# Kernel tuning notes

Hardware: AMD Instinct MI355X
Metric: run time of the kernel (lower is better)

Reference implementation:

```python
import jax, jax.numpy as jnp
import numpy as np

K = 32  # num_nearest_neighbors

def silu(x):
    return x * jax.nn.sigmoid(x)

def setup_inputs() -> dict:
    key = jax.random.key(0)
    ks = jax.random.split(key, 10)
    b, n, d, m = 4, 2048, 64, 16
    e_in = 2 * d + 1  # 129 = fourier*2 + dim*2 + edge_dim + 1
    std = 0.001  # init_eps normal init on Linear weights
    inp = {
        "feats": jax.random.normal(ks[0], (b, n, d), dtype=jnp.float32),
        "coors": jax.random.normal(ks[1], (b, n, 3), dtype=jnp.float32),
        # edge_mlp: Linear(129,258) -> SiLU -> Linear(258,16) -> SiLU
        "ew1": jax.random.normal(ks[2], (e_in, 2 * e_in), dtype=jnp.float32) * std,
        "eb1": jnp.zeros((2 * e_in,), dtype=jnp.float32),
        "ew2": jax.random.normal(ks[3], (2 * e_in, m), dtype=jnp.float32) * std,
        "eb2": jnp.zeros((m,), dtype=jnp.float32),
        # coors_mlp: Linear(16,64) -> SiLU -> Linear(64,1)
        "cw1": jax.random.normal(ks[4], (m, 4 * m), dtype=jnp.float32) * std,
        "cb1": jnp.zeros((4 * m,), dtype=jnp.float32),
        "cw2": jax.random.normal(ks[5], (4 * m, 1), dtype=jnp.float32) * std,
        "cb2": jnp.zeros((1,), dtype=jnp.float32),
        # node_mlp: Linear(80,128) -> SiLU -> Linear(128,64)
        "nw1": jax.random.normal(ks[6], (d + m, 2 * d), dtype=jnp.float32) * std,
        "nb1": jnp.zeros((2 * d,), dtype=jnp.float32),
        "nw2": jax.random.normal(ks[7], (2 * d, d), dtype=jnp.float32) * std,
        "nb2": jnp.zeros((d,), dtype=jnp.float32),
    }
    return inp


def reference(feats, coors, ew1, eb1, ew2, eb2, cw1, cb1, cw2, cb2, nw1, nb1, nw2, nb2):
    b, n, d = feats.shape
    # pairwise relative coords / squared distances: [b,n,n,3], [b,n,n]
    rel = coors[:, :, None, :] - coors[:, None, :, :]
    dist2 = jnp.sum(rel * rel, axis=-1)
    # k nearest neighbors (smallest squared distance)
    _, idx = jax.lax.top_k(-dist2, K)  # idx: [b,n,K]
    bi = jnp.arange(b)[:, None, None]
    ii = jnp.arange(n)[None, :, None]
    rel_k = rel[bi, ii, idx]                # [b,n,K,3]
    dist_k = dist2[bi, ii, idx][..., None]  # [b,n,K,1]
    feats_j = feats[bi, idx]                # [b,n,K,d]
    feats_i = jnp.broadcast_to(feats[:, :, None, :], feats_j.shape)
    # edge MLP
    edge_in = jnp.concatenate([feats_i, feats_j, dist_k], axis=-1)  # [b,n,K,2d+1]
    h = silu(edge_in @ ew1 + eb1)
    m_ij = silu(h @ ew2 + eb2)  # [b,n,K,m]
    # coordinate update
    coor_w = (silu(m_ij @ cw1 + cb1) @ cw2 + cb2)[..., 0]  # [b,n,K]
    coors_out = jnp.einsum('bik,bikc->bic', coor_w, rel_k) + coors
    # node update (sum pooling over neighbors)
    m_i = jnp.sum(m_ij, axis=-2)  # [b,n,m]
    node_in = jnp.concatenate([feats, m_i], axis=-1)
    node_out = silu(node_in @ nw1 + nb1) @ nw2 + nb2 + feats
    return (node_out, coors_out)
```

## Files before the change

kernel.cpp:

```cpp
#include <hip/hip_runtime.h>
#include <math.h>

#define NB 4
#define NN 2048
#define ND 64
#define NM 16
#define NK 32
#define EIN 129
#define EH 258
#define CHD 64
#define NHD 128
#define PQS 288
#define XS 96
#define KNN_BLOCKS (NB * NN / 4)
#define PREP_BLOCKS 92

typedef __attribute__((ext_vector_type(8))) short short8;
typedef __attribute__((ext_vector_type(4))) float f32x4;
typedef __attribute__((ext_vector_type(4))) int intx4;

__device__ __forceinline__ float fast_silu(float x) {
    return x * __builtin_amdgcn_rcpf(1.f + __expf(-x));
}

__device__ __forceinline__ short f2bf(float f) {
    union { float f; unsigned u; } v; v.f = f;
    unsigned r = v.u + 0x7FFFu + ((v.u >> 16) & 1u);
    return (short)(r >> 16);
}

__device__ __forceinline__ float bf2f(short s) {
    union { unsigned u; float f; } v;
    v.u = ((unsigned)(unsigned short)s) << 16;
    return v.f;
}

__device__ __forceinline__ unsigned cvt_pk_bf16(float lo, float hi) {
    unsigned r;
    asm("v_cvt_pk_bf16_f32 %0, %1, %2" : "=v"(r) : "v"(lo), "v"(hi));
    return r;
}

__device__ __forceinline__ unsigned umin_u(unsigned a, unsigned b) { return a < b ? a : b; }
__device__ __forceinline__ unsigned umax_u(unsigned a, unsigned b) { return a > b ? a : b; }

__global__ __launch_bounds__(256) void pk_kernel(
    const float* __restrict__ coors, int* __restrict__ idx_out,
    const float* __restrict__ ew1, const float* __restrict__ ew2, const float* __restrict__ eb1,
    const float* __restrict__ cw1,
    const float* __restrict__ nw1, const float* __restrict__ nw2,
    float* __restrict__ w1pad, float* __restrict__ eb1pad,
    short* __restrict__ W2T, short* __restrict__ W1F, short* __restrict__ cw1T,
    short* __restrict__ nw1F, short* __restrict__ nw2F) {
    const int tid = threadIdx.x;

    if (blockIdx.x >= KNN_BLOCKS) {
        const int blk = blockIdx.x - KNN_BLOCKS;
        if (blk < 72) {
            const int kk = blk & 1, ct = (blk >> 1) % 18, half = blk / 36;
            for (int t = tid; t < 512; t += 256) {
                const int l = t >> 3, i = t & 7;
                const int er = l & 15, grp = l >> 4;
                const int k = kk * 32 + grp * 8 + i;
                const int col = ct * 16 + er;
                const int row = half * 64 + k;
                W1F[blk * 512 + t] = (col < EH) ? f2bf(ew1[row * EH + col]) : (short)0;
            }
        } else if (blk == 72) {
            for (int c = tid; c < PQS; c += 256) {
                w1pad[c] = (c < EH) ? ew1[128 * EH + c] : 0.f;
                eb1pad[c] = (c < EH) ? eb1[c] : 0.f;
            }
        } else if (blk < 89) {
            const int t = blk - 73;
            for (int k = tid; k < PQS; k += 256)
                W2T[t * PQS + k] = (k < EH) ? f2bf(ew2[k * NM + t]) : (short)0;
        } else if (blk == 89) {
            for (int t2 = tid; t2 < CHD * NM; t2 += 256) {
                const int h = t2 >> 4, t = t2 & 15;
                cw1T[t2] = f2bf(cw1[t * CHD + h]);
            }
        } else if (blk == 90) {
            for (int t = tid; t < 24 * 512; t += 256) {
                const int f = t >> 9, t2 = t & 511;
                const int ct = f / 3, kk = f % 3;
                const int l = t2 >> 3, i = t2 & 7;
                const int er = l & 15, grp = l >> 4;
                const int k = kk * 32 + grp * 8 + i;
                const int col = ct * 16 + er;
                nw1F[t] = (k < 80) ? f2bf(nw1[k * NHD + col]) : (short)0;
            }
        } else {
            for (int t = tid; t < 16 * 512; t += 256) {
                const int f = t >> 9, t2 = t & 511;
                const int ct = f >> 2, kk = f & 3;
                const int l = t2 >> 3, i = t2 & 7;
                const int er = l & 15, grp = l >> 4;
                const int k = kk * 32 + grp * 8 + i;
                const int col = ct * 16 + er;
                nw2F[t] = f2bf(nw2[k * ND + col]);
            }
        }
        return;
    }

    const int wg = ((blockIdx.x & 7) << 8) | (blockIdx.x >> 3);
    const int wv = tid >> 6;
    const int lane = tid & 63;
    const int row = wg * 4 + wv;
    const int b = row >> 11;
    const int i = row & (NN - 1);
    const float* cb = coors + (size_t)b * NN * 3;
    const float cix = cb[i * 3 + 0], ciy = cb[i * 3 + 1], ciz = cb[i * 3 + 2];

    unsigned k[32];
    #pragma unroll
    for (int t = 0; t < 32; ++t) {
        int j = lane + 64 * t;
        const float* cj = cb + (size_t)j * 3;
        float dx = cix - cj[0];
        float dy = ciy - cj[1];
        float dz = ciz - cj[2];
        float d = dx * dx + dy * dy + dz * dz;
        union { float f; unsigned u; } v; v.f = d;
        k[t] = (v.u & 0xFFFFF800u) | (unsigned)j;
    }

    #pragma unroll
    for (int size = 2; size <= 32; size <<= 1) {
        #pragma unroll
        for (int stride = size >> 1; stride > 0; stride >>= 1) {
            #pragma unroll
            for (int t = 0; t < 32; ++t) {
                int p = t ^ stride;
                if (p > t) {
                    const bool up = ((t & size) == 0);
                    unsigned lo = umin_u(k[t], k[p]);
                    unsigned hi = umax_u(k[t], k[p]);
                    k[t] = up ? lo : hi;
                    k[p] = up ? hi : lo;
                }
            }
        }
    }

    #pragma unroll
    for (int off = 1; off < 64; off <<= 1) {
        unsigned pr[32];
        #pragma unroll
        for (int t = 0; t < 32; ++t) pr[t] = __shfl_xor(k[31 - t], off);
        #pragma unroll
        for (int t = 0; t < 32; ++t) k[t] = umin_u(k[t], pr[t]);
        #pragma unroll
        for (int s = 16; s > 0; s >>= 1) {
            #pragma unroll
            for (int t = 0; t < 32; ++t) {
                if ((t & s) == 0) {
                    const int p = t | s;
                    unsigned lo = umin_u(k[t], k[p]);
                    unsigned hi = umax_u(k[t], k[p]);
                    k[t] = lo; k[p] = hi;
                }
            }
        }
    }

    if (lane == 0) {
        intx4* op = (intx4*)(idx_out + (size_t)row * NK);
        #pragma unroll
        for (int q = 0; q < 8; ++q) {
            intx4 v;
            v[0] = (int)(k[q * 4 + 0] & 2047u);
            v[1] = (int)(k[q * 4 + 1] & 2047u);
            v[2] = (int)(k[q * 4 + 2] & 2047u);
            v[3] = (int)(k[q * 4 + 3] & 2047u);
            op[q] = v;
        }
    }
}

__global__ __launch_bounds__(256) void pq_kernel(const float* __restrict__ feats,
                                                 const short* __restrict__ W1F,
                                                 const float* __restrict__ eb1pad,
                                                 short* __restrict__ P,
                                                 short* __restrict__ Q,
                                                 short* __restrict__ xbuf) {
    const int wv = threadIdx.x >> 6, lane = threadIdx.x & 63;
    const int er = lane & 15, grp = lane >> 4;
    const int wid = blockIdx.x * 4 + wv;
    const int mt = wid / 18, ct = wid % 18;
    const int nb = mt * 16;

    short8 a[2];
    #pragma unroll
    for (int kk = 0; kk < 2; ++kk) {
        const float* fp = feats + (size_t)(nb + er) * ND + kk * 32 + grp * 8;
        f32x4 f0 = *(const f32x4*)fp;
        f32x4 f1 = *(const f32x4*)(fp + 4);
        union { intx4 iv; short8 s; } u;
        u.iv[0] = cvt_pk_bf16(f0[0], f0[1]);
        u.iv[1] = cvt_pk_bf16(f0[2], f0[3]);
        u.iv[2] = cvt_pk_bf16(f1[0], f1[1]);
        u.iv[3] = cvt_pk_bf16(f1[2], f1[3]);
        a[kk] = u.s;
    }

    if (ct == 0) {
        short* xr = xbuf + (size_t)(nb + er) * XS;
        *(short8*)(xr + 0 * 32 + grp * 8) = a[0];
        *(short8*)(xr + 1 * 32 + grp * 8) = a[1];
        if (grp == 0) {
            const short8 z8 = {0, 0, 0, 0, 0, 0, 0, 0};
            *(short8*)(xr + 80) = z8;
            *(short8*)(xr + 88) = z8;
        }
    }

    const short8* WF = (const short8*)W1F;
    short8 bP0 = WF[((0 * 18 + ct) * 2 + 0) * 64 + lane];
    short8 bP1 = WF[((0 * 18 + ct) * 2 + 1) * 64 + lane];
    short8 bQ0 = WF[((1 * 18 + ct) * 2 + 0) * 64 + lane];
    short8 bQ1 = WF[((1 * 18 + ct) * 2 + 1) * 64 + lane];

    f32x4 accP = {0.f, 0.f, 0.f, 0.f};
    f32x4 accQ = {0.f, 0.f, 0.f, 0.f};
    accP = __builtin_amdgcn_mfma_f32_16x16x32_bf16(a[0], bP0, accP, 0, 0, 0);
    accP = __builtin_amdgcn_mfma_f32_16x16x32_bf16(a[1], bP1, accP, 0, 0, 0);
    accQ = __builtin_amdgcn_mfma_f32_16x16x32_bf16(a[0], bQ0, accQ, 0, 0, 0);
    accQ = __builtin_amdgcn_mfma_f32_16x16x32_bf16(a[1], bQ1, accQ, 0, 0, 0);

    const float bias = eb1pad[ct * 16 + er];
    #pragma unroll
    for (int r = 0; r < 4; ++r) {
        const int node = nb + grp * 4 + r;
        P[(size_t)node * PQS + ct * 16 + er] = f2bf(accP[r] + bias);
        Q[(size_t)node * PQS + ct * 16 + er] = f2bf(accQ[r]);
    }
}

__global__ __launch_bounds__(256) void edge_kernel(
    const float* __restrict__ coors, const int* __restrict__ idx,
    const short* __restrict__ P, const short* __restrict__ Q,
    const float* __restrict__ w1pad, const short* __restrict__ W2T,
    const float* __restrict__ eb2,
    const short* __restrict__ cw1T, const float* __restrict__ cb1,
    const float* __restrict__ cw2, const float* __restrict__ cb2,
    float* __restrict__ coors_out, short* __restrict__ xbuf) {

    __shared__ __align__(16) short mtl[4][NK][NM];

    const int tid = threadIdx.x;
    const int wg = ((blockIdx.x & 7) << 8) | (blockIdx.x >> 3);
    const int wv = tid >> 6, lane = tid & 63;
    const int er = lane & 15, grp = lane >> 4;
    const int gi = wg * 4 + wv;
    const int b = gi >> 11;

    const int j0 = idx[gi * NK + er];
    const int j1 = idx[gi * NK + 16 + er];
    const float ci0 = coors[gi * 3 + 0], ci1 = coors[gi * 3 + 1], ci2 = coors[gi * 3 + 2];
    const float* cj0p = coors + (size_t)(b * NN + j0) * 3;
    const float* cj1p = coors + (size_t)(b * NN + j1) * 3;
    const float r0x = ci0 - cj0p[0], r0y = ci1 - cj0p[1], r0z = ci2 - cj0p[2];
    const float r1x = ci0 - cj1p[0], r1y = ci1 - cj1p[1], r1z = ci2 - cj1p[2];
    const float d0 = r0x * r0x + r0y * r0y + r0z * r0z;
    const float d1 = r1x * r1x + r1y * r1y + r1z * r1z;

    const short8* Pr8 = (const short8*)(P + (size_t)gi * PQS);
    const short8* Q0 = (const short8*)(Q + (size_t)(b * NN + j0) * PQS);
    const short8* Q1 = (const short8*)(Q + (size_t)(b * NN + j1) * PQS);
    const short8* w2row = (const short8*)(W2T + er * PQS);
    const f32x4* w14 = (const f32x4*)w1pad;

    short8 qb0a[9], qb1a[9];
    #pragma unroll
    for (int kk = 0; kk < 9; ++kk) {
        qb0a[kk] = Q0[kk * 4 + grp];
        qb1a[kk] = Q1[kk * 4 + grp];
    }

    f32x4 acc0 = {0.f, 0.f, 0.f, 0.f};
    f32x4 acc1 = {0.f, 0.f, 0.f, 0.f};
    #pragma unroll
    for (int kk = 0; kk < 9; ++kk) {
        short8 bf = w2row[kk * 4 + grp];
        short8 pb = Pr8[kk * 4 + grp];
        f32x4 w0 = w14[kk * 8 + grp * 2];
        f32x4 w1 = w14[kk * 8 + grp * 2 + 1];
        float wf[8] = {w0[0], w0[1], w0[2], w0[3], w1[0], w1[1], w1[2], w1[3]};
        float pf[8];
        #pragma unroll
        for (int i = 0; i < 8; ++i) pf[i] = bf2f(pb[i]);
        float h0[8], h1[8];
        #pragma unroll
        for (int i = 0; i < 8; ++i) {
            h0[i] = fast_silu(fmaf(d0, wf[i], pf[i]) + bf2f(qb0a[kk][i]));
            h1[i] = fast_silu(fmaf(d1, wf[i], pf[i]) + bf2f(qb1a[kk][i]));
        }
        union { intx4 iv; short8 s; } u0, u1;
        u0.iv[0] = cvt_pk_bf16(h0[0], h0[1]);
        u0.iv[1] = cvt_pk_bf16(h0[2], h0[3]);
        u0.iv[2] = cvt_pk_bf16(h0[4], h0[5]);
        u0.iv[3] = cvt_pk_bf16(h0[6], h0[7]);
        u1.iv[0] = cvt_pk_bf16(h1[0], h1[1]);
        u1.iv[1] = cvt_pk_bf16(h1[2], h1[3]);
        u1.iv[2] = cvt_pk_bf16(h1[4], h1[5]);
        u1.iv[3] = cvt_pk_bf16(h1[6], h1[7]);
        acc0 = __builtin_amdgcn_mfma_f32_16x16x32_bf16(u0.s, bf, acc0, 0, 0, 0);
        acc1 = __builtin_amdgcn_mfma_f32_16x16x32_bf16(u1.s, bf, acc1, 0, 0, 0);
    }

    const float eb2v = eb2[er];
    float m0[4], m1[4];
    #pragma unroll
    for (int r = 0; r < 4; ++r) {
        m0[r] = fast_silu(acc0[r] + eb2v);
        m1[r] = fast_silu(acc1[r] + eb2v);
    }

    float s = m0[0] + m0[1] + m0[2] + m0[3] + m1[0] + m1[1] + m1[2] + m1[3];
    s += __shfl_xor(s, 16);
    s += __shfl_xor(s, 32);
    if (lane < NM) xbuf[(size_t)gi * XS + ND + er] = f2bf(s);

    #pragma unroll
    for (int r = 0; r < 4; ++r) {
        mtl[wv][grp * 4 + r][er] = f2bf(m0[r]);
        mtl[wv][16 + grp * 4 + r][er] = f2bf(m1[r]);
    }
    __syncthreads();

    const short8 zero8 = {0, 0, 0, 0, 0, 0, 0, 0};
    short8 afr[4];
    #pragma unroll
    for (int mt = 0; mt < 4; ++mt)
        afr[mt] = (grp < 2) ? *(const short8*)(cw1T + (mt * 16 + er) * NM + grp * 8) : zero8;

    float cwv[2];
    #pragma unroll
    for (int nt = 0; nt < 2; ++nt) {
        short8 bfr = (grp < 2) ? *(const short8*)&mtl[wv][nt * 16 + er][grp * 8] : zero8;
        float partial = 0.f;
        #pragma unroll
        for (int mt = 0; mt < 4; ++mt) {
            f32x4 dz = {0.f, 0.f, 0.f, 0.f};
            dz = __builtin_amdgcn_mfma_f32_16x16x32_bf16(afr[mt], bfr, dz, 0, 0, 0);
            f32x4 cb1v = *(const f32x4*)(cb1 + mt * 16 + grp * 4);
            f32x4 cw2v = *(const f32x4*)(cw2 + mt * 16 + grp * 4);
            #pragma unroll
            for (int r = 0; r < 4; ++r)
                partial += fast_silu(dz[r] + cb1v[r]) * cw2v[r];
        }
        partial += __shfl_xor(partial, 16);
        partial += __shfl_xor(partial, 32);
        cwv[nt] = partial + cb2[0];
    }

    float wx = cwv[0] * r0x + cwv[1] * r1x;
    float wy = cwv[0] * r0y + cwv[1] * r1y;
    float wz = cwv[0] * r0z + cwv[1] * r1z;
    #pragma unroll
    for (int off = 1; off < 16; off <<= 1) {
        wx += __shfl_xor(wx, off);
        wy += __shfl_xor(wy, off);
        wz += __shfl_xor(wz, off);
    }
    if (lane == 0) {
        coors_out[gi * 3 + 0] = ci0 + wx;
        coors_out[gi * 3 + 1] = ci1 + wy;
        coors_out[gi * 3 + 2] = ci2 + wz;
    }
}

__global__ __launch_bounds__(256) void node_kernel(
    const short* __restrict__ xbuf,
    const short* __restrict__ nw1F, const float* __restrict__ nb1,
    const short* __restrict__ nw2F, const float* __restrict__ nb2,
    const float* __restrict__ feats, float* __restrict__ node_out) {
    __shared__ __align__(16) short hl[16 * 128];
    const int tid = threadIdx.x;
    const int wv = tid >> 6, lane = tid & 63;
    const int er = lane & 15, grp = lane >> 4;
    const int nb = blockIdx.x * 16;

    short8 a[3];
    #pragma unroll
    for (int kk = 0; kk < 3; ++kk)
        a[kk] = *(const short8*)(xbuf + (size_t)(nb + er) * XS + kk * 32 + grp * 8);

    #pragma unroll
    for (int c2 = 0; c2 < 2; ++c2) {
        const int ct = wv * 2 + c2;
        f32x4 acc = {0.f, 0.f, 0.f, 0.f};
        #pragma unroll
        for (int kk = 0; kk < 3; ++kk)
            acc = __builtin_amdgcn_mfma_f32_16x16x32_bf16(
                a[kk], *(const short8*)(nw1F + (ct * 3 + kk) * 512 + lane * 8), acc, 0, 0, 0);
        const float b1 = nb1[ct * 16 + er];
        #pragma unroll
        for (int r = 0; r < 4; ++r) {
            const int row = grp * 4 + r;
            int byte = row * 256 + (ct * 16 + er) * 2;
            byte ^= (row & 7) << 4;
            *(short*)((char*)hl + byte) = f2bf(fast_silu(acc[r] + b1));
        }
    }
    __syncthreads();

    short8 a2[4];
    #pragma unroll
    for (int kk = 0; kk < 4; ++kk) {
        int byte = er * 256 + kk * 64 + grp * 16;
        byte ^= (er & 7) << 4;
        a2[kk] = *(const short8*)((const char*)hl + byte);
    }
    f32x4 acc = {0.f, 0.f, 0.f, 0.f};
    #pragma unroll
    for (int kk = 0; kk < 4; ++kk)
        acc = __builtin_amdgcn_mfma_f32_16x16x32_bf16(
            a2[kk], *(const short8*)(nw2F + (wv * 4 + kk) * 512 + lane * 8), acc, 0, 0, 0);
    const float b2 = nb2[wv * 16 + er];
    #pragma unroll
    for (int r = 0; r < 4; ++r) {
        const int node = nb + grp * 4 + r;
        node_out[(size_t)node * ND + wv * 16 + er] =
            acc[r] + b2 + feats[(size_t)node * ND + wv * 16 + er];
    }
}

extern "C" void kernel_launch(void* const* d_in, const int* in_sizes, int n_in,
                              void* d_out, int out_size, void* d_ws, size_t ws_size,
                              hipStream_t stream) {
    const float* feats = (const float*)d_in[0];
    const float* coors = (const float*)d_in[1];
    const float* ew1 = (const float*)d_in[2];
    const float* eb1 = (const float*)d_in[3];
    const float* ew2 = (const float*)d_in[4];
    const float* eb2 = (const float*)d_in[5];
    const float* cw1 = (const float*)d_in[6];
    const float* cb1 = (const float*)d_in[7];
    const float* cw2 = (const float*)d_in[8];
    const float* cb2 = (const float*)d_in[9];
    const float* nw1 = (const float*)d_in[10];
    const float* nb1 = (const float*)d_in[11];
    const float* nw2 = (const float*)d_in[12];
    const float* nb2 = (const float*)d_in[13];

    float* out_node = (float*)d_out;
    float* out_coors = out_node + (size_t)NB * NN * ND;

    char* ws = (char*)d_ws;
    int*   idx    = (int*)(ws + 0);
    short* P      = (short*)(ws + 1048576);
    short* Q      = (short*)(ws + 5767168);
    float* w1pad  = (float*)(ws + 10485760);
    float* eb1pad = (float*)(ws + 10486912);
    short* W2T    = (short*)(ws + 10488064);
    short* W1F    = (short*)(ws + 10497280);
    short* cw1T   = (short*)(ws + 10571008);
    short* nw1F   = (short*)(ws + 10573056);
    short* nw2F   = (short*)(ws + 10597632);
    short* xbuf   = (short*)(ws + 10614016);

    pk_kernel<<<KNN_BLOCKS + PREP_BLOCKS, 256, 0, stream>>>(
        coors, idx, ew1, ew2, eb1, cw1, nw1, nw2,
        w1pad, eb1pad, W2T, W1F, cw1T, nw1F, nw2F);
    pq_kernel<<<(512 * 18) / 4, 256, 0, stream>>>(feats, W1F, eb1pad, P, Q, xbuf);
    edge_kernel<<<NB * NN / 4, 256, 0, stream>>>(
        coors, idx, P, Q, w1pad, W2T, eb2, cw1T, cb1, cw2, cb2,
        out_coors, xbuf);
    node_kernel<<<NB * NN / 16, 256, 0, stream>>>(
        xbuf, nw1F, nb1, nw2F, nb2, feats, out_node);
}
```

Before: 91.62 us.

## Fuse PQ projection into KNN kernel and use DPP shuffles in merge

Merges the P/Q edge-projection GEMM into the KNN launch by interleaving PQ blocks with KNN blocks, so one kernel launch and its dependency gap go away. The PQ blocks now read and convert ew1 weights straight from global memory instead of a pre-packed W1F buffer. In the bitonic merge across lanes, xor-1 and xor-2 exchanges use DPP moves, the reverse-and-min step is done in place, and the final re-sort after the last merge level is skipped. It also sets an occupancy hint of 8 blocks per SM. In exchange, the weight loads are strided and uncoalesced and repeated by every PQ wave.

```diff
diff --git a/kernel.cpp b/kernel.cpp
--- a/kernel.cpp
+++ b/kernel.cpp
@@ -12,8 +12,10 @@
 #define NHD 128
 #define PQS 288
 #define XS 96
-#define KNN_BLOCKS (NB * NN / 4)
-#define PREP_BLOCKS 92
+#define KNN_BLOCKS 2048
+#define PQ_BLOCKS 2304
+#define PREP_BLOCKS 20
+#define TOTAL_BLOCKS (4096 + 256 + PREP_BLOCKS)
 
 typedef __attribute__((ext_vector_type(8))) short short8;
 typedef __attribute__((ext_vector_type(4))) float f32x4;
@@ -44,43 +46,41 @@
 __device__ __forceinline__ unsigned umin_u(unsigned a, unsigned b) { return a < b ? a : b; }
 __device__ __forceinline__ unsigned umax_u(unsigned a, unsigned b) { return a > b ? a : b; }
 
-__global__ __launch_bounds__(256) void pk_kernel(
+__device__ __forceinline__ unsigned shx1(unsigned x) {
+    return (unsigned)__builtin_amdgcn_mov_dpp((int)x, 0xB1, 0xF, 0xF, true);
+}
+__device__ __forceinline__ unsigned shx2(unsigned x) {
+    return (unsigned)__builtin_amdgcn_mov_dpp((int)x, 0x4E, 0xF, 0xF, true);
+}
+
+__global__ __launch_bounds__(256, 8) void pk_kernel(
     const float* __restrict__ coors, int* __restrict__ idx_out,
+    const float* __restrict__ feats,
     const float* __restrict__ ew1, const float* __restrict__ ew2, const float* __restrict__ eb1,
     const float* __restrict__ cw1,
     const float* __restrict__ nw1, const float* __restrict__ nw2,
-    float* __restrict__ w1pad, float* __restrict__ eb1pad,
-    short* __restrict__ W2T, short* __restrict__ W1F, short* __restrict__ cw1T,
-    short* __restrict__ nw1F, short* __restrict__ nw2F) {
+    float* __restrict__ w1pad,
+    short* __restrict__ W2T, short* __restrict__ cw1T,
+    short* __restrict__ nw1F, short* __restrict__ nw2F,
+    short* __restrict__ P, short* __restrict__ Q, short* __restrict__ xbuf) {
     const int tid = threadIdx.x;
-
-    if (blockIdx.x >= KNN_BLOCKS) {
-        const int blk = blockIdx.x - KNN_BLOCKS;
-        if (blk < 72) {
-            const int kk = blk & 1, ct = (blk >> 1) % 18, half = blk / 36;
-            for (int t = tid; t < 512; t += 256) {
-                const int l = t >> 3, i = t & 7;
-                const int er = l & 15, grp = l >> 4;
-                const int k = kk * 32 + grp * 8 + i;
-                const int col = ct * 16 + er;
-                const int row = half * 64 + k;
-                W1F[blk * 512 + t] = (col < EH) ? f2bf(ew1[row * EH + col]) : (short)0;
-            }
-        } else if (blk == 72) {
-            for (int c = tid; c < PQS; c += 256) {
+    const int B = blockIdx.x;
+
+    if (B >= 4352) {
+        const int blk = B - 4352;
+        if (blk == 0) {
+            for (int c = tid; c < PQS; c += 256)
                 w1pad[c] = (c < EH) ? ew1[128 * EH + c] : 0.f;
-                eb1pad[c] = (c < EH) ? eb1[c] : 0.f;
-            }
-        } else if (blk < 89) {
-            const int t = blk - 73;
+        } else if (blk <= 16) {
+            const int t = blk - 1;
             for (int k = tid; k < PQS; k += 256)
                 W2T[t * PQS + k] = (k < EH) ? f2bf(ew2[k * NM + t]) : (short)0;
-        } else if (blk == 89) {
+        } else if (blk == 17) {
             for (int t2 = tid; t2 < CHD * NM; t2 += 256) {
                 const int h = t2 >> 4, t = t2 & 15;
                 cw1T[t2] = f2bf(cw1[t * CHD + h]);
             }
-        } else if (blk == 90) {
+        } else if (blk == 18) {
             for (int t = tid; t < 24 * 512; t += 256) {
                 const int f = t >> 9, t2 = t & 511;
                 const int ct = f / 3, kk = f % 3;
@@ -104,9 +104,74 @@
         return;
     }
 
-    const int wg = ((blockIdx.x & 7) << 8) | (blockIdx.x >> 3);
+    bool is_pq; int sub;
+    if (B < 4096) { is_pq = (B & 1); sub = B >> 1; }
+    else { is_pq = true; sub = 2048 + (B - 4096); }
+
     const int wv = tid >> 6;
     const int lane = tid & 63;
+    const int er = lane & 15, grp = lane >> 4;
+
+    if (is_pq) {
+        const int wid = sub * 4 + wv;
+        const int mt = wid / 18, ct = wid % 18;
+        const int nb = mt * 16;
+
+        short8 a[2];
+        #pragma unroll
+        for (int kk = 0; kk < 2; ++kk) {
+            const float* fp = feats + (size_t)(nb + er) * ND + kk * 32 + grp * 8;
+            f32x4 f0 = *(const f32x4*)fp;
+            f32x4 f1 = *(const f32x4*)(fp + 4);
+            union { intx4 iv; short8 s; } u;
+            u.iv[0] = cvt_pk_bf16(f0[0], f0[1]);
+            u.iv[1] = cvt_pk_bf16(f0[2], f0[3]);
+            u.iv[2] = cvt_pk_bf16(f1[0], f1[1]);
+            u.iv[3] = cvt_pk_bf16(f1[2], f1[3]);
+            a[kk] = u.s;
+        }
+
+        if (ct == 0) {
+            short* xr = xbuf + (size_t)(nb + er) * XS;
+            *(short8*)(xr + 0 * 32 + grp * 8) = a[0];
+            *(short8*)(xr + 1 * 32 + grp * 8) = a[1];
+            if (grp == 0) {
+                const short8 z8 = {0, 0, 0, 0, 0, 0, 0, 0};
+                *(short8*)(xr + 80) = z8;
+                *(short8*)(xr + 88) = z8;
+            }
+        }
+
+        const int col = ct * 16 + er;
+        const bool cok = (col < EH);
+        short8 bP0, bP1, bQ0, bQ1;
+        #pragma unroll
+        for (int i = 0; i < 8; ++i) {
+            const int rr = grp * 8 + i;
+            bP0[i] = cok ? f2bf(ew1[(size_t)(rr) * EH + col]) : (short)0;
+            bP1[i] = cok ? f2bf(ew1[(size_t)(32 + rr) * EH + col]) : (short)0;
+            bQ0[i] = cok ? f2bf(ew1[(size_t)(64 + rr) * EH + col]) : (short)0;
+            bQ1[i] = cok ? f2bf(ew1[(size_t)(96 + rr) * EH + col]) : (short)0;
+        }
+
+        f32x4 accP = {0.f, 0.f, 0.f, 0.f};
+        f32x4 accQ = {0.f, 0.f, 0.f, 0.f};
+        accP = __builtin_amdgcn_mfma_f32_16x16x32_bf16(a[0], bP0, accP, 0, 0, 0);
+        accP = __builtin_amdgcn_mfma_f32_16x16x32_bf16(a[1], bP1, accP, 0, 0, 0);
+        accQ = __builtin_amdgcn_mfma_f32_16x16x32_bf16(a[0], bQ0, accQ, 0, 0, 0);
+        accQ = __builtin_amdgcn_mfma_f32_16x16x32_bf16(a[1], bQ1, accQ, 0, 0, 0);
+
+        const float bias = cok ? eb1[col] : 0.f;
+        #pragma unroll
+        for (int r = 0; r < 4; ++r) {
+            const int node = nb + grp * 4 + r;
+            P[(size_t)node * PQS + col] = f2bf(accP[r] + bias);
+            Q[(size_t)node * PQS + col] = f2bf(accQ[r]);
+        }
+        return;
+    }
+
+    const int wg = ((sub & 7) << 8) | (sub >> 3);
     const int row = wg * 4 + wv;
     const int b = row >> 11;
     const int i = row & (NN - 1);
@@ -146,20 +211,27 @@
 
     #pragma unroll
     for (int off = 1; off < 64; off <<= 1) {
-        unsigned pr[32];
-        #pragma unroll
-        for (int t = 0; t < 32; ++t) pr[t] = __shfl_xor(k[31 - t], off);
-        #pragma unroll
-        for (int t = 0; t < 32; ++t) k[t] = umin_u(k[t], pr[t]);
-        #pragma unroll
-        for (int s = 16; s > 0; s >>= 1) {
+        #pragma unroll
+        for (int t = 0; t < 16; ++t) {
+            const int u = 31 - t;
+            unsigned pa, pb;
+            if (off == 1) { pa = shx1(k[u]); pb = shx1(k[t]); }
+            else if (off == 2) { pa = shx2(k[u]); pb = shx2(k[t]); }
+            else { pa = __shfl_xor(k[u], off); pb = __shfl_xor(k[t], off); }
+            k[t] = umin_u(k[t], pa);
+            k[u] = umin_u(k[u], pb);
+        }
+        if (off < 32) {
             #pragma unroll
-            for (int t = 0; t < 32; ++t) {
-                if ((t & s) == 0) {
-                    const int p = t | s;
-                    unsigned lo = umin_u(k[t], k[p]);
-                    unsigned hi = umax_u(k[t], k[p]);
-                    k[t] = lo; k[p] = hi;
+            for (int s = 16; s > 0; s >>= 1) {
+                #pragma unroll
+                for (int t = 0; t < 32; ++t) {
+                    if ((t & s) == 0) {
+                        const int p = t | s;
+                        unsigned lo = umin_u(k[t], k[p]);
+                        unsigned hi = umax_u(k[t], k[p]);
+                        k[t] = lo; k[p] = hi;
+                    }
                 }
             }
         }
@@ -176,65 +248,6 @@
             v[3] = (int)(k[q * 4 + 3] & 2047u);
             op[q] = v;
         }
-    }
-}
-
-__global__ __launch_bounds__(256) void pq_kernel(const float* __restrict__ feats,
-                                                 const short* __restrict__ W1F,
-                                                 const float* __restrict__ eb1pad,
-                                                 short* __restrict__ P,
-                                                 short* __restrict__ Q,
-                                                 short* __restrict__ xbuf) {
-    const int wv = threadIdx.x >> 6, lane = threadIdx.x & 63;
-    const int er = lane & 15, grp = lane >> 4;
-    const int wid = blockIdx.x * 4 + wv;
-    const int mt = wid / 18, ct = wid % 18;
-    const int nb = mt * 16;
-
-    short8 a[2];
-    #pragma unroll
-    for (int kk = 0; kk < 2; ++kk) {
-        const float* fp = feats + (size_t)(nb + er) * ND + kk * 32 + grp * 8;
-        f32x4 f0 = *(const f32x4*)fp;
-        f32x4 f1 = *(const f32x4*)(fp + 4);
-        union { intx4 iv; short8 s; } u;
-        u.iv[0] = cvt_pk_bf16(f0[0], f0[1]);
-        u.iv[1] = cvt_pk_bf16(f0[2], f0[3]);
-        u.iv[2] = cvt_pk_bf16(f1[0], f1[1]);
-        u.iv[3] = cvt_pk_bf16(f1[2], f1[3]);
-        a[kk] = u.s;
-    }
-
-    if (ct == 0) {
-        short* xr = xbuf + (size_t)(nb + er) * XS;
-        *(short8*)(xr + 0 * 32 + grp * 8) = a[0];
-        *(short8*)(xr + 1 * 32 + grp * 8) = a[1];
-        if (grp == 0) {
-            const short8 z8 = {0, 0, 0, 0, 0, 0, 0, 0};
-            *(short8*)(xr + 80) = z8;
-            *(short8*)(xr + 88) = z8;
-        }
-    }
-
-    const short8* WF = (const short8*)W1F;
-    short8 bP0 = WF[((0 * 18 + ct) * 2 + 0) * 64 + lane];
-    short8 bP1 = WF[((0 * 18 + ct) * 2 + 1) * 64 + lane];
-    short8 bQ0 = WF[((1 * 18 + ct) * 2 + 0) * 64 + lane];
-    short8 bQ1 = WF[((1 * 18 + ct) * 2 + 1) * 64 + lane];
-
-    f32x4 accP = {0.f, 0.f, 0.f, 0.f};
-    f32x4 accQ = {0.f, 0.f, 0.f, 0.f};
-    accP = __builtin_amdgcn_mfma_f32_16x16x32_bf16(a[0], bP0, accP, 0, 0, 0);
-    accP = __builtin_amdgcn_mfma_f32_16x16x32_bf16(a[1], bP1, accP, 0, 0, 0);
-    accQ = __builtin_amdgcn_mfma_f32_16x16x32_bf16(a[0], bQ0, accQ, 0, 0, 0);
-    accQ = __builtin_amdgcn_mfma_f32_16x16x32_bf16(a[1], bQ1, accQ, 0, 0, 0);
-
-    const float bias = eb1pad[ct * 16 + er];
-    #pragma unroll
-    for (int r = 0; r < 4; ++r) {
-        const int node = nb + grp * 4 + r;
-        P[(size_t)node * PQS + ct * 16 + er] = f2bf(accP[r] + bias);
-        Q[(size_t)node * PQS + ct * 16 + er] = f2bf(accQ[r]);
     }
 }
 
@@ -454,18 +467,15 @@
     short* P      = (short*)(ws + 1048576);
     short* Q      = (short*)(ws + 5767168);
     float* w1pad  = (float*)(ws + 10485760);
-    float* eb1pad = (float*)(ws + 10486912);
-    short* W2T    = (short*)(ws + 10488064);
-    short* W1F    = (short*)(ws + 10497280);
-    short* cw1T   = (short*)(ws + 10571008);
-    short* nw1F   = (short*)(ws + 10573056);
-    short* nw2F   = (short*)(ws + 10597632);
-    short* xbuf   = (short*)(ws + 10614016);
-
-    pk_kernel<<<KNN_BLOCKS + PREP_BLOCKS, 256, 0, stream>>>(
-        coors, idx, ew1, ew2, eb1, cw1, nw1, nw2,
-        w1pad, eb1pad, W2T, W1F, cw1T, nw1F, nw2F);
-    pq_kernel<<<(512 * 18) / 4, 256, 0, stream>>>(feats, W1F, eb1pad, P, Q, xbuf);
+    short* W2T    = (short*)(ws + 10486912);
+    short* cw1T   = (short*)(ws + 10496128);
+    short* nw1F   = (short*)(ws + 10498176);
+    short* nw2F   = (short*)(ws + 10522752);
+    short* xbuf   = (short*)(ws + 10539136);
+
+    pk_kernel<<<TOTAL_BLOCKS, 256, 0, stream>>>(
+        coors, idx, feats, ew1, ew2, eb1, cw1, nw1, nw2,
+        w1pad, W2T, cw1T, nw1F, nw2F, P, Q, xbuf);
     edge_kernel<<<NB * NN / 4, 256, 0, stream>>>(
         coors, idx, P, Q, w1pad, W2T, eb2, cw1T, cb1, cw2, cb2,
         out_coors, xbuf);
```

Result: slower. 104.1 us (+13.6%).

## Fuse node MLP into edge kernel, removing node kernel and xbuf round-trip

Applied to the files above, without the earlier changes.

Moves the node MLP into the tail of the edge kernel. Each block's four nodes keep their features and pooled messages in shared memory instead of writing a bf16 staging buffer to global memory and launching a separate node kernel. This saves one kernel launch and the global write and read of xbuf. In exchange, each block runs 16-row MFMA tiles with only 4 valid rows, wasting three quarters of the matrix work, and adds shared memory and a barrier to the edge kernel, which may lower occupancy.

```diff
diff --git a/kernel.cpp b/kernel.cpp
--- a/kernel.cpp
+++ b/kernel.cpp
@@ -12,7 +12,7 @@
 #define NHD 128
 #define PQS 288
 #define XS 96
-#define KNN_BLOCKS (NB * NN / 4)
+#define KNN_BLOCKS 2048
 #define PREP_BLOCKS 92
 
 typedef __attribute__((ext_vector_type(8))) short short8;
@@ -104,7 +104,8 @@
         return;
     }
 
-    const int wg = ((blockIdx.x & 7) << 8) | (blockIdx.x >> 3);
+    const int sub = blockIdx.x;
+    const int wg = ((sub & 7) << 8) | (sub >> 3);
     const int wv = tid >> 6;
     const int lane = tid & 63;
     const int row = wg * 4 + wv;
@@ -183,8 +184,7 @@
                                                  const short* __restrict__ W1F,
                                                  const float* __restrict__ eb1pad,
                                                  short* __restrict__ P,
-                                                 short* __restrict__ Q,
-                                                 short* __restrict__ xbuf) {
+                                                 short* __restrict__ Q) {
     const int wv = threadIdx.x >> 6, lane = threadIdx.x & 63;
     const int er = lane & 15, grp = lane >> 4;
     const int wid = blockIdx.x * 4 + wv;
@@ -205,17 +205,6 @@
         a[kk] = u.s;
     }
 
-    if (ct == 0) {
-        short* xr = xbuf + (size_t)(nb + er) * XS;
-        *(short8*)(xr + 0 * 32 + grp * 8) = a[0];
-        *(short8*)(xr + 1 * 32 + grp * 8) = a[1];
-        if (grp == 0) {
-            const short8 z8 = {0, 0, 0, 0, 0, 0, 0, 0};
-            *(short8*)(xr + 80) = z8;
-            *(short8*)(xr + 88) = z8;
-        }
-    }
-
     const short8* WF = (const short8*)W1F;
     short8 bP0 = WF[((0 * 18 + ct) * 2 + 0) * 64 + lane];
     short8 bP1 = WF[((0 * 18 + ct) * 2 + 1) * 64 + lane];
@@ -245,16 +234,24 @@
     const float* __restrict__ eb2,
     const short* __restrict__ cw1T, const float* __restrict__ cb1,
     const float* __restrict__ cw2, const float* __restrict__ cb2,
-    float* __restrict__ coors_out, short* __restrict__ xbuf) {
+    const float* __restrict__ feats,
+    const short* __restrict__ nw1F, const float* __restrict__ nb1,
+    const short* __restrict__ nw2F, const float* __restrict__ nb2,
+    float* __restrict__ coors_out, float* __restrict__ node_out) {
 
     __shared__ __align__(16) short mtl[4][NK][NM];
+    __shared__ float xs[4][80];
+    __shared__ __align__(16) short hl[16 * 128];
 
     const int tid = threadIdx.x;
     const int wg = ((blockIdx.x & 7) << 8) | (blockIdx.x >> 3);
     const int wv = tid >> 6, lane = tid & 63;
     const int er = lane & 15, grp = lane >> 4;
-    const int gi = wg * 4 + wv;
+    const int gbase = wg * 4;
+    const int gi = gbase + wv;
     const int b = gi >> 11;
+
+    xs[wv][lane] = feats[(size_t)gi * ND + lane];
 
     const int j0 = idx[gi * NK + er];
     const int j1 = idx[gi * NK + 16 + er];
@@ -321,7 +318,7 @@
     float s = m0[0] + m0[1] + m0[2] + m0[3] + m1[0] + m1[1] + m1[2] + m1[3];
     s += __shfl_xor(s, 16);
     s += __shfl_xor(s, 32);
-    if (lane < NM) xbuf[(size_t)gi * XS + ND + er] = f2bf(s);
+    if (lane < NM) xs[wv][ND + er] = s;
 
     #pragma unroll
     for (int r = 0; r < 4; ++r) {
@@ -370,23 +367,27 @@
         coors_out[gi * 3 + 1] = ci1 + wy;
         coors_out[gi * 3 + 2] = ci2 + wz;
     }
-}
-
-__global__ __launch_bounds__(256) void node_kernel(
-    const short* __restrict__ xbuf,
-    const short* __restrict__ nw1F, const float* __restrict__ nb1,
-    const short* __restrict__ nw2F, const float* __restrict__ nb2,
-    const float* __restrict__ feats, float* __restrict__ node_out) {
-    __shared__ __align__(16) short hl[16 * 128];
-    const int tid = threadIdx.x;
-    const int wv = tid >> 6, lane = tid & 63;
-    const int er = lane & 15, grp = lane >> 4;
-    const int nb = blockIdx.x * 16;
-
-    short8 a[3];
-    #pragma unroll
-    for (int kk = 0; kk < 3; ++kk)
-        a[kk] = *(const short8*)(xbuf + (size_t)(nb + er) * XS + kk * 32 + grp * 8);
+
+    short8 na[3];
+    #pragma unroll
+    for (int kk = 0; kk < 3; ++kk) {
+        if (er < 4) {
+            float xv[8];
+            #pragma unroll
+            for (int i = 0; i < 8; ++i) {
+                const int kx = kk * 32 + grp * 8 + i;
+                xv[i] = (kx < 80) ? xs[er][kx] : 0.f;
+            }
+            union { intx4 iv; short8 sv; } u;
+            u.iv[0] = cvt_pk_bf16(xv[0], xv[1]);
+            u.iv[1] = cvt_pk_bf16(xv[2], xv[3]);
+            u.iv[2] = cvt_pk_bf16(xv[4], xv[5]);
+            u.iv[3] = cvt_pk_bf16(xv[6], xv[7]);
+            na[kk] = u.sv;
+        } else {
+            na[kk] = zero8;
+        }
+    }
 
     #pragma unroll
     for (int c2 = 0; c2 < 2; ++c2) {
@@ -395,14 +396,15 @@
         #pragma unroll
         for (int kk = 0; kk < 3; ++kk)
             acc = __builtin_amdgcn_mfma_f32_16x16x32_bf16(
-                a[kk], *(const short8*)(nw1F + (ct * 3 + kk) * 512 + lane * 8), acc, 0, 0, 0);
+                na[kk], *(const short8*)(nw1F + (ct * 3 + kk) * 512 + lane * 8), acc, 0, 0, 0);
         const float b1 = nb1[ct * 16 + er];
-        #pragma unroll
-        for (int r = 0; r < 4; ++r) {
-            const int row = grp * 4 + r;
-            int byte = row * 256 + (ct * 16 + er) * 2;
-            byte ^= (row & 7) << 4;
-            *(short*)((char*)hl + byte) = f2bf(fast_silu(acc[r] + b1));
+        if (grp == 0) {
+            #pragma unroll
+            for (int r = 0; r < 4; ++r) {
+                int byte = r * 256 + (ct * 16 + er) * 2;
+                byte ^= (r & 7) << 4;
+                *(short*)((char*)hl + byte) = f2bf(fast_silu(acc[r] + b1));
+            }
         }
     }
     __syncthreads();
@@ -410,9 +412,13 @@
     short8 a2[4];
     #pragma unroll
     for (int kk = 0; kk < 4; ++kk) {
-        int byte = er * 256 + kk * 64 + grp * 16;
-        byte ^= (er & 7) << 4;
-        a2[kk] = *(const short8*)((const char*)hl + byte);
+        if (er < 4) {
+            int byte = er * 256 + kk * 64 + grp * 16;
+            byte ^= (er & 7) << 4;
+            a2[kk] = *(const short8*)((const char*)hl + byte);
+        } else {
+            a2[kk] = zero8;
+        }
     }
     f32x4 acc = {0.f, 0.f, 0.f, 0.f};
     #pragma unroll
@@ -420,11 +426,13 @@
         acc = __builtin_amdgcn_mfma_f32_16x16x32_bf16(
             a2[kk], *(const short8*)(nw2F + (wv * 4 + kk) * 512 + lane * 8), acc, 0, 0, 0);
     const float b2 = nb2[wv * 16 + er];
-    #pragma unroll
-    for (int r = 0; r < 4; ++r) {
-        const int node = nb + grp * 4 + r;
-        node_out[(size_t)node * ND + wv * 16 + er] =
-            acc[r] + b2 + feats[(size_t)node * ND + wv * 16 + er];
+    if (grp == 0) {
+        #pragma unroll
+        for (int r = 0; r < 4; ++r) {
+            const int node = gbase + r;
+            node_out[(size_t)node * ND + wv * 16 + er] =
+                acc[r] + b2 + feats[(size_t)node * ND + wv * 16 + er];
+        }
     }
 }
 
@@ -460,15 +468,12 @@
     short* cw1T   = (short*)(ws + 10571008);
     short* nw1F   = (short*)(ws + 10573056);
     short* nw2F   = (short*)(ws + 10597632);
-    short* xbuf   = (short*)(ws + 10614016);
 
     pk_kernel<<<KNN_BLOCKS + PREP_BLOCKS, 256, 0, stream>>>(
         coors, idx, ew1, ew2, eb1, cw1, nw1, nw2,
         w1pad, eb1pad, W2T, W1F, cw1T, nw1F, nw2F);
-    pq_kernel<<<(512 * 18) / 4, 256, 0, stream>>>(feats, W1F, eb1pad, P, Q, xbuf);
+    pq_kernel<<<(512 * 18) / 4, 256, 0, stream>>>(feats, W1F, eb1pad, P, Q);
     edge_kernel<<<NB * NN / 4, 256, 0, stream>>>(
         coors, idx, P, Q, w1pad, W2T, eb2, cw1T, cb1, cw2, cb2,
-        out_coors, xbuf);
-    node_kernel<<<NB * NN / 16, 256, 0, stream>>>(
-        xbuf, nw1F, nb1, nw2F, nb2, feats, out_node);
-}
+        feats, nw1F, nb1, nw2F, nb2, out_coors, out_node);
+}
```

Measured after the change: 90.44 us. No clear change (-1.3%).
